# Kernel tuning notes

Measured on AMD Instinct MI355X. Metric: run time of the kernel, lower is better.

## Reference

```python
import jax, jax.numpy as jnp
import numpy as np
import itertools


def _identity_grid(n, d, h, w, dtype):
    # Replicates AffineGridGenerator with identity theta:
    # linspace(-1,1,K) per axis (align_corners=True convention),
    # grid[..., 0]=x(W), grid[...,1]=y(H), grid[...,2]=z(D).
    zs = jnp.linspace(-1.0, 1.0, d, dtype=dtype) if d > 1 else jnp.array([-1.0], dtype=dtype)
    ys = jnp.linspace(-1.0, 1.0, h, dtype=dtype) if h > 1 else jnp.array([-1.0], dtype=dtype)
    xs = jnp.linspace(-1.0, 1.0, w, dtype=dtype) if w > 1 else jnp.array([-1.0], dtype=dtype)
    gz, gy, gx = jnp.meshgrid(zs, ys, xs, indexing='ij')  # [D,H,W]
    grid = jnp.stack([gx, gy, gz], axis=-1)               # [D,H,W,3]
    return jnp.broadcast_to(grid, (n, d, h, w, 3))


def _trilinear_sample(x, grid):
    N, C, Din, Hin, Win = x.shape
    dt = x.dtype
    fx = (grid[..., 0] + 1.0) * 0.5 * (Win - 1)
    fy = (grid[..., 1] + 1.0) * 0.5 * (Hin - 1)
    fz = (grid[..., 2] + 1.0) * 0.5 * (Din - 1)
    x0 = jnp.floor(fx); y0 = jnp.floor(fy); z0 = jnp.floor(fz)
    wx1 = (fx - x0).astype(dt); wy1 = (fy - y0).astype(dt); wz1 = (fz - z0).astype(dt)
    wx = (1.0 - wx1, wx1); wy = (1.0 - wy1, wy1); wz = (1.0 - wz1, wz1)
    ix = (x0.astype(jnp.int32), x0.astype(jnp.int32) + 1)
    iy = (y0.astype(jnp.int32), y0.astype(jnp.int32) + 1)
    iz = (z0.astype(jnp.int32), z0.astype(jnp.int32) + 1)

    def gather(xb, izb, iyb, ixb):
        return xb[:, izb, iyb, ixb]  # [C,D,H,W]
    gather_b = jax.vmap(gather)

    out = jnp.zeros((N, C) + grid.shape[1:4], dtype=dt)
    for a, b, c in itertools.product((0, 1), repeat=3):  # (z,y,x) corner
        zi, yi, xi = iz[a], iy[b], ix[c]
        valid = ((zi >= 0) & (zi < Din) & (yi >= 0) & (yi < Hin)
                 & (xi >= 0) & (xi < Win))
        zi = jnp.clip(zi, 0, Din - 1)
        yi = jnp.clip(yi, 0, Hin - 1)
        xi = jnp.clip(xi, 0, Win - 1)
        wgt = (wz[a] * wy[b] * wx[c]) * valid.astype(dt)  # [N,D,H,W]
        vals = gather_b(x, zi, yi, xi)                     # [N,C,D,H,W]
        out = out + vals * wgt[:, None]
    return out


def reference(x, d_out, h_out, w_out, variance):
    if variance:
        x = jnp.exp(x / 2.0)
    grid = _identity_grid(x.shape[0], d_out, h_out, w_out, x.dtype)
    out = _trilinear_sample(x, grid)
    if variance:
        out = jnp.log(out) * 2.0
    return out


def setup_inputs() -> dict:
    key = jax.random.key(0)
    x = jax.random.normal(key, (8, 32, 32, 64, 64), dtype=jnp.float32)
    return {"x": x, "d_out": 48, "h_out": 96, "w_out": 96, "variance": 1}
```

## Files before the change

kernel.cpp:

```cpp
#include <hip/hip_runtime.h>

constexpr int N = 8, C = 32, Din = 32, Hin = 64, Win = 64;
constexpr int Do = 48, Ho = 96, Wo = 96;

constexpr int BLOCK   = 256;
constexpr int NBLOCKS = N * C * Do;
constexpr int GPAD    = 68;

typedef float f32x4 __attribute__((ext_vector_type(4)));

__global__ __launch_bounds__(BLOCK)
void resample3d_var_kernel(const float* __restrict__ in, float* __restrict__ out) {
    __shared__ float G[Hin][GPAD];

    const int tid = threadIdx.x;
    const int bid = blockIdx.x;
    const int zo  = bid % Do;
    const int nc  = bid / Do;

    float fz  = (float)(zo * (Din - 1)) * (1.0f / (float)(Do - 1));
    int   z0  = (int)fz;
    float wz1 = fz - (float)z0;
    int   z1  = min(z0 + 1, Din - 1);
    float wz0 = 1.0f - wz1;

    const float* __restrict__ p0 = in + ((size_t)nc * Din + z0) * (Hin * Win);
    const float* __restrict__ p1 = in + ((size_t)nc * Din + z1) * (Hin * Win);

    constexpr float HALF_LOG2E = 0.7213475204444817f;

    {
        const int sy = tid >> 4;
        const int sx = (tid & 15) << 2;
#pragma unroll
        for (int k = 0; k < 4; ++k) {
            int y = sy + k * 16;
            const float4 a = *reinterpret_cast<const float4*>(p0 + y * Win + sx);
            const float4 b = *reinterpret_cast<const float4*>(p1 + y * Win + sx);
            float4 g;
            g.x = wz0 * __builtin_amdgcn_exp2f(a.x * HALF_LOG2E) + wz1 * __builtin_amdgcn_exp2f(b.x * HALF_LOG2E);
            g.y = wz0 * __builtin_amdgcn_exp2f(a.y * HALF_LOG2E) + wz1 * __builtin_amdgcn_exp2f(b.y * HALF_LOG2E);
            g.z = wz0 * __builtin_amdgcn_exp2f(a.z * HALF_LOG2E) + wz1 * __builtin_amdgcn_exp2f(b.z * HALF_LOG2E);
            g.w = wz0 * __builtin_amdgcn_exp2f(a.w * HALF_LOG2E) + wz1 * __builtin_amdgcn_exp2f(b.w * HALF_LOG2E);
            *reinterpret_cast<float4*>(&G[y][sx]) = g;
        }
    }
    __syncthreads();

    float* __restrict__ ob = out + ((size_t)nc * Do + zo) * (size_t)(Ho * Wo);
    constexpr float TWO_LN2 = 1.3862943611198906f;

#pragma unroll 3
    for (int k = 0; k < 9; ++k) {
        int c   = k * BLOCK + tid;
        int row = (c * 2731) >> 16;
        int q   = c - row * 24;

        float fy  = (float)(row * (Hin - 1)) * (1.0f / (float)(Ho - 1));
        int   y0  = (int)fy;
        float wy1 = fy - (float)y0;
        int   y1  = min(y0 + 1, Hin - 1);
        const float* __restrict__ g0 = &G[y0][0];
        const float* __restrict__ g1 = &G[y1][0];

        f32x4 o;
#pragma unroll
        for (int i = 0; i < 4; ++i) {
            int   xo  = q * 4 + i;
            float fx  = (float)(xo * (Win - 1)) * (1.0f / (float)(Wo - 1));
            int   x0  = (int)fx;
            float wx1 = fx - (float)x0;
            int   x1  = min(x0 + 1, Win - 1);
            float a0 = g0[x0], a1 = g0[x1];
            float b0 = g1[x0], b1 = g1[x1];
            float fa = a0 + wy1 * (b0 - a0);
            float fb = a1 + wy1 * (b1 - a1);
            float v  = fa + wx1 * (fb - fa);
            o[i] = TWO_LN2 * __log2f(v);
        }
        __builtin_nontemporal_store(o, reinterpret_cast<f32x4*>(ob + (size_t)c * 4));
    }
}

extern "C" void kernel_launch(void* const* d_in, const int* in_sizes, int n_in,
                              void* d_out, int out_size, void* d_ws, size_t ws_size,
                              hipStream_t stream) {
    const float* x = (const float*)d_in[0];
    float* out = (float*)d_out;
    resample3d_var_kernel<<<NBLOCKS, BLOCK, 0, stream>>>(x, out);
}
```

Baseline: 137.1 us.

## Split resample into per-wave row chunks with register double-buffered loads, no block barrier

Each wavefront now owns 24 output rows and processes them in three chunks of 8. It loads the needed input rows straight from global into registers, applies the z and y interpolation in registers, and stages only x-line values in a per-wave shared buffer. The next chunk's loads are issued before the current chunk is consumed, so load latency overlaps compute, and the block-wide __syncthreads goes away. The cost is redundant exp evaluation and global loads (rows are refetched per output row instead of once per input row), more register pressure under a 5-wave occupancy hint, and plain stores replacing nontemporal ones. Shared-buffer reuse within a wave relies on lockstep execution with no explicit wave barrier.

```diff
diff --git a/kernel.cpp b/kernel.cpp
--- a/kernel.cpp
+++ b/kernel.cpp
@@ -2,84 +2,101 @@
 
 constexpr int N = 8, C = 32, Din = 32, Hin = 64, Win = 64;
 constexpr int Do = 48, Ho = 96, Wo = 96;
-
-constexpr int BLOCK   = 256;
-constexpr int NBLOCKS = N * C * Do;
-constexpr int GPAD    = 68;
+constexpr int BLOCK = 256, NBLOCKS = N * C * Do;
+constexpr int RPC = 8;
+constexpr int PAD = 68;
 
 typedef float f32x4 __attribute__((ext_vector_type(4)));
 
-__global__ __launch_bounds__(BLOCK)
+__global__ __launch_bounds__(BLOCK, 5)
 void resample3d_var_kernel(const float* __restrict__ in, float* __restrict__ out) {
-    __shared__ float G[Hin][GPAD];
+    __shared__ float F2[4][RPC][PAD];
 
-    const int tid = threadIdx.x;
-    const int bid = blockIdx.x;
-    const int zo  = bid % Do;
-    const int nc  = bid / Do;
+    const int tid  = threadIdx.x;
+    const int w    = tid >> 6;
+    const int lane = tid & 63;
+    const int bid  = blockIdx.x;
+    const int zo   = bid % Do;
+    const int nc   = bid / Do;
 
     float fz  = (float)(zo * (Din - 1)) * (1.0f / (float)(Do - 1));
     int   z0  = (int)fz;
     float wz1 = fz - (float)z0;
     int   z1  = min(z0 + 1, Din - 1);
-    float wz0 = 1.0f - wz1;
 
     const float* __restrict__ p0 = in + ((size_t)nc * Din + z0) * (Hin * Win);
     const float* __restrict__ p1 = in + ((size_t)nc * Din + z1) * (Hin * Win);
 
+    const int r0w = w * 24;
+    float* __restrict__ ob = out + ((size_t)nc * Do + zo) * (size_t)(Ho * Wo);
+
     constexpr float HALF_LOG2E = 0.7213475204444817f;
+    constexpr float TWO_LN2    = 1.3862943611198906f;
 
-    {
-        const int sy = tid >> 4;
-        const int sx = (tid & 15) << 2;
-#pragma unroll
-        for (int k = 0; k < 4; ++k) {
-            int y = sy + k * 16;
-            const float4 a = *reinterpret_cast<const float4*>(p0 + y * Win + sx);
-            const float4 b = *reinterpret_cast<const float4*>(p1 + y * Win + sx);
-            float4 g;
-            g.x = wz0 * __builtin_amdgcn_exp2f(a.x * HALF_LOG2E) + wz1 * __builtin_amdgcn_exp2f(b.x * HALF_LOG2E);
-            g.y = wz0 * __builtin_amdgcn_exp2f(a.y * HALF_LOG2E) + wz1 * __builtin_amdgcn_exp2f(b.y * HALF_LOG2E);
-            g.z = wz0 * __builtin_amdgcn_exp2f(a.z * HALF_LOG2E) + wz1 * __builtin_amdgcn_exp2f(b.z * HALF_LOG2E);
-            g.w = wz0 * __builtin_amdgcn_exp2f(a.w * HALF_LOG2E) + wz1 * __builtin_amdgcn_exp2f(b.w * HALF_LOG2E);
-            *reinterpret_cast<float4*>(&G[y][sx]) = g;
-        }
+    float a0[RPC], a1[RPC], b0[RPC], b1[RPC];
+    float c0[RPC], c1[RPC], d0[RPC], d1[RPC];
+
+#define LOADCH(ch, A0, A1, B0, B1)                                     \
+    _Pragma("unroll")                                                  \
+    for (int j = 0; j < RPC; ++j) {                                    \
+        int   yo = r0w + (ch) * RPC + j;                               \
+        float fy = (float)(yo * (Hin - 1)) * (1.0f / (float)(Ho - 1)); \
+        int   y0 = (int)fy;                                            \
+        int   y1 = min(y0 + 1, Hin - 1);                               \
+        A0[j] = p0[y0 * Win + lane];                                   \
+        A1[j] = p0[y1 * Win + lane];                                   \
+        B0[j] = p1[y0 * Win + lane];                                   \
+        B1[j] = p1[y1 * Win + lane];                                   \
     }
-    __syncthreads();
 
-    float* __restrict__ ob = out + ((size_t)nc * Do + zo) * (size_t)(Ho * Wo);
-    constexpr float TWO_LN2 = 1.3862943611198906f;
+#define STAGECH(ch, A0, A1, B0, B1)                                    \
+    _Pragma("unroll")                                                  \
+    for (int j = 0; j < RPC; ++j) {                                    \
+        int   yo  = r0w + (ch) * RPC + j;                              \
+        float fy  = (float)(yo * (Hin - 1)) * (1.0f / (float)(Ho - 1));\
+        float wy1 = fy - (float)(int)fy;                               \
+        float e00 = __builtin_amdgcn_exp2f(A0[j] * HALF_LOG2E);        \
+        float e01 = __builtin_amdgcn_exp2f(A1[j] * HALF_LOG2E);        \
+        float e10 = __builtin_amdgcn_exp2f(B0[j] * HALF_LOG2E);        \
+        float e11 = __builtin_amdgcn_exp2f(B1[j] * HALF_LOG2E);        \
+        float f0  = e00 + wy1 * (e01 - e00);                           \
+        float f1  = e10 + wy1 * (e11 - e10);                           \
+        F2[w][j][lane] = f0 + wz1 * (f1 - f0);                         \
+    }
 
-#pragma unroll 3
-    for (int k = 0; k < 9; ++k) {
-        int c   = k * BLOCK + tid;
-        int row = (c * 2731) >> 16;
-        int q   = c - row * 24;
+#define CONSUMECH(ch)                                                  \
+    _Pragma("unroll")                                                  \
+    for (int i = 0; i < 3; ++i) {                                      \
+        int t   = i * 64 + lane;                                       \
+        int row = (t * 2731) >> 16;        \
+        int q   = t - row * 24;                                        \
+        f32x4 o;                                                       \
+        _Pragma("unroll")                                              \
+        for (int ii = 0; ii < 4; ++ii) {                               \
+            int   xo  = q * 4 + ii;                                    \
+            float fx  = (float)(xo * (Win - 1)) * (1.0f / (float)(Wo - 1)); \
+            int   x0  = (int)fx;                                       \
+            float wx1 = fx - (float)x0;                                \
+            int   x1  = min(x0 + 1, Win - 1);                          \
+            float F0 = F2[w][row][x0], F1 = F2[w][row][x1];            \
+            o[ii] = TWO_LN2 * __log2f(F0 + wx1 * (F1 - F0));           \
+        }                                                              \
+        *reinterpret_cast<f32x4*>(ob + ((r0w + (ch) * RPC) * Wo) + t * 4) = o; \
+    }
 
-        float fy  = (float)(row * (Hin - 1)) * (1.0f / (float)(Ho - 1));
-        int   y0  = (int)fy;
-        float wy1 = fy - (float)y0;
-        int   y1  = min(y0 + 1, Hin - 1);
-        const float* __restrict__ g0 = &G[y0][0];
-        const float* __restrict__ g1 = &G[y1][0];
+    LOADCH(0, a0, a1, b0, b1)
+    STAGECH(0, a0, a1, b0, b1)
+    LOADCH(1, c0, c1, d0, d1)
+    CONSUMECH(0)
+    STAGECH(1, c0, c1, d0, d1)
+    LOADCH(2, a0, a1, b0, b1)
+    CONSUMECH(1)
+    STAGECH(2, a0, a1, b0, b1)
+    CONSUMECH(2)
 
-        f32x4 o;
-#pragma unroll
-        for (int i = 0; i < 4; ++i) {
-            int   xo  = q * 4 + i;
-            float fx  = (float)(xo * (Win - 1)) * (1.0f / (float)(Wo - 1));
-            int   x0  = (int)fx;
-            float wx1 = fx - (float)x0;
-            int   x1  = min(x0 + 1, Win - 1);
-            float a0 = g0[x0], a1 = g0[x1];
-            float b0 = g1[x0], b1 = g1[x1];
-            float fa = a0 + wy1 * (b0 - a0);
-            float fb = a1 + wy1 * (b1 - a1);
-            float v  = fa + wx1 * (fb - fa);
-            o[i] = TWO_LN2 * __log2f(v);
-        }
-        __builtin_nontemporal_store(o, reinterpret_cast<f32x4*>(ob + (size_t)c * 4));
-    }
+#undef LOADCH
+#undef STAGECH
+#undef CONSUMECH
 }
 
 extern "C" void kernel_launch(void* const* d_in, const int* in_sizes, int n_in,
```

Result: slower. 161.9 us (+18.1%).
